# Kernel tuning notes

Hardware: AMD Instinct MI355X
Metric: run time of the kernel (lower is better)

## Reference

```python
import jax, jax.numpy as jnp
import numpy as np

RANK = 16
ALPHA = 32.0


def setup_inputs() -> dict:
    key = jax.random.key(0)
    k1, k2, k3, k4, k5 = jax.random.split(key, 5)
    B_, S, D = 8, 2048, 2048
    x = jax.random.normal(k1, (B_, S, D), dtype=jnp.float32)
    W = jax.random.normal(k2, (D, D), dtype=jnp.float32) * 0.02  # linear.weight [out, in]
    b = jax.random.normal(k3, (D,), dtype=jnp.float32) * 0.02
    # LoRA init: B ~ N(0, 1/rank), A = 0 in the original; use randn*std for both so grads flow
    std = 1.0 / np.sqrt(RANK)
    B = jax.random.normal(k4, (D, RANK), dtype=jnp.float32) * std
    A = jax.random.normal(k5, (RANK, D), dtype=jnp.float32) * 0.02
    return {"x": x, "W": W, "b": b, "B": B, "A": A}


def reference(x, W, b, B, A):
    # delta_w = B @ A  -> [in, out] (== [out, in] since square)
    delta_w = jnp.matmul(B, A)
    w = W + (ALPHA / RANK) * delta_w
    # F.linear(x, w, b) = x @ w.T + b
    return jnp.einsum("bsd,od->bso", x, w) + b
```

## Files before the change

### kernel.cpp

```cpp
#include <hip/hip_runtime.h>
#include <hip/hip_bf16.h>

typedef unsigned short u16;
typedef __bf16 bf16x8 __attribute__((ext_vector_type(8)));
typedef float f32x4 __attribute__((ext_vector_type(4)));

#define MDIM 16384
#define NDIM 2048
#define KDIM 2048
#define RANK 16
#define BM 128
#define BN 128
#define BK 64

#define WPREP_BLOCKS (NDIM * (KDIM / 4) / 256)
#define XCONV_BLOCKS (MDIM * (KDIM / 4) / 256)

__device__ __forceinline__ u16 f2bf(float f) {
    union { float f; unsigned u; } v; v.f = f;
    unsigned u = v.u;
    u += 0x7FFFu + ((u >> 16) & 1u);
    return (u16)(u >> 16);
}

__device__ __forceinline__ void async_copy16(const void* gsrc, void* ldst) {
    __builtin_amdgcn_global_load_lds(
        (const __attribute__((address_space(1))) void*)gsrc,
        (__attribute__((address_space(3))) void*)ldst,
        16, 0, 0);
}

__global__ __launch_bounds__(256) void prep(const float* __restrict__ x,
                                            const float* __restrict__ W,
                                            const float* __restrict__ Bm,
                                            const float* __restrict__ Am,
                                            u16* __restrict__ xb,
                                            u16* __restrict__ wb) {
    const int bid = blockIdx.x;
    if (bid < WPREP_BLOCKS) {
        int t  = bid * 256 + threadIdx.x;
        int o  = t >> 9;
        int dq = t & 511;
        float4 acc = ((const float4*)W)[(size_t)o * (KDIM / 4) + dq];
        const float* Bo = Bm + (size_t)o * RANK;
#pragma unroll
        for (int r = 0; r < RANK; ++r) {
            float bv = 2.0f * Bo[r];
            float4 a4 = ((const float4*)(Am + (size_t)r * KDIM))[dq];
            acc.x += bv * a4.x; acc.y += bv * a4.y;
            acc.z += bv * a4.z; acc.w += bv * a4.w;
        }
        ushort4 ov;
        ov.x = f2bf(acc.x); ov.y = f2bf(acc.y);
        ov.z = f2bf(acc.z); ov.w = f2bf(acc.w);
        ((ushort4*)wb)[t] = ov;
    } else {
        int t = (bid - WPREP_BLOCKS) * 256 + threadIdx.x;
        float4 v = ((const float4*)x)[t];
        ushort4 o;
        o.x = f2bf(v.x); o.y = f2bf(v.y); o.z = f2bf(v.z); o.w = f2bf(v.w);
        ((ushort4*)xb)[t] = o;
    }
}

__global__ __launch_bounds__(256) void gemm_bt(const u16* __restrict__ xb,
                                               const u16* __restrict__ wb,
                                               const float* __restrict__ bias,
                                               float* __restrict__ out) {
    __shared__ __align__(16) u16 As[BM * BK];
    __shared__ __align__(16) u16 Bs[BN * BK];

    const int tid  = threadIdx.x;
    const int lane = tid & 63;
    const int w    = tid >> 6;
    const int m0   = blockIdx.y * BM;
    const int n0   = blockIdx.x * BN;

    const int srow   = lane >> 3;
    const int schunk = (lane & 7) ^ srow;
    const int selem  = schunk * 8;

    const int wr   = (w >> 1) * 64;
    const int wc   = (w & 1) * 64;
    const int quad = lane >> 4;
    const int l16  = lane & 15;
    const int swz  = l16 & 7;

    int a_row[4], b_row[4];
#pragma unroll
    for (int i = 0; i < 4; ++i) {
        a_row[i] = (wr + i * 16 + l16) * BK;
        b_row[i] = (wc + i * 16 + l16) * BK;
    }

    f32x4 acc[4][4];
#pragma unroll
    for (int i = 0; i < 4; ++i)
#pragma unroll
        for (int j = 0; j < 4; ++j)
            acc[i][j] = (f32x4){0.f, 0.f, 0.f, 0.f};

    const u16* ga = xb + (size_t)m0 * KDIM;
    const u16* gb = wb + (size_t)n0 * KDIM;

    for (int k0 = 0; k0 < KDIM; k0 += BK) {
#pragma unroll
        for (int c = 0; c < 4; ++c) {
            const int rbase = w * 32 + c * 8;
            async_copy16(ga + (size_t)(rbase + srow) * KDIM + k0 + selem,
                         (char*)As + (size_t)rbase * (BK * 2));
            async_copy16(gb + (size_t)(rbase + srow) * KDIM + k0 + selem,
                         (char*)Bs + (size_t)rbase * (BK * 2));
        }
        __syncthreads();

#pragma unroll
        for (int s = 0; s < 2; ++s) {
            bf16x8 af[4], bfr[4];
#pragma unroll
            for (int i = 0; i < 4; ++i)
                af[i]  = *(const bf16x8*)(As + a_row[i] + (((s * 4 + quad) ^ swz) << 3));
#pragma unroll
            for (int j = 0; j < 4; ++j)
                bfr[j] = *(const bf16x8*)(Bs + b_row[j] + (((s * 4 + quad) ^ swz) << 3));

#pragma unroll
            for (int i = 0; i < 4; ++i)
#pragma unroll
                for (int j = 0; j < 4; ++j)
                    acc[i][j] = __builtin_amdgcn_mfma_f32_16x16x32_bf16(
                        af[i], bfr[j], acc[i][j], 0, 0, 0);
        }

        __syncthreads();
    }

#pragma unroll
    for (int j = 0; j < 4; ++j) {
        const int col = n0 + wc + j * 16 + l16;
        const float bj = bias[col];
#pragma unroll
        for (int i = 0; i < 4; ++i) {
            const int rowb = m0 + wr + i * 16 + quad * 4;
#pragma unroll
            for (int r = 0; r < 4; ++r)
                out[(size_t)(rowb + r) * NDIM + col] = acc[i][j][r] + bj;
        }
    }
}

extern "C" void kernel_launch(void* const* d_in, const int* in_sizes, int n_in,
                              void* d_out, int out_size, void* d_ws, size_t ws_size,
                              hipStream_t stream) {
    const float* x    = (const float*)d_in[0];
    const float* W    = (const float*)d_in[1];
    const float* bias = (const float*)d_in[2];
    const float* Bm   = (const float*)d_in[3];
    const float* Am   = (const float*)d_in[4];
    float* out = (float*)d_out;

    u16* xb   = (u16*)d_ws;
    u16* wbuf = xb + (size_t)MDIM * KDIM;

    prep<<<WPREP_BLOCKS + XCONV_BLOCKS, 256, 0, stream>>>(x, W, Bm, Am, xb, wbuf);

    dim3 grid(NDIM / BN, MDIM / BM);
    gemm_bt<<<grid, 256, 0, stream>>>(xb, wbuf, bias, out);
}
```

Baseline: 401.0 us.

## Rewrite GEMM with 256x256 tiles, double-buffered LDS pipeline and XCD-aware block mapping

The bf16 GEMM moves from 128x128 tiles with 256 threads and a single LDS buffer to 256x256 tiles with 512 threads (8 waves, each computing 128x64). Global-to-LDS async copies are double-buffered and interleaved with four MFMA phases per K-tile, using explicit barriers, waitcnt and setprio so loads overlap compute. A 1D grid is remapped so consecutive blocks are spread across XCDs for L2 reuse. This removes the load-then-compute stall and raises arithmetic intensity per tile. In exchange it costs more registers and 128KB of LDS per block, and the hand-scheduled waitcnt and barrier ordering is delicate.

```diff
diff --git a/kernel.cpp b/kernel.cpp
--- a/kernel.cpp
+++ b/kernel.cpp
@@ -9,9 +9,11 @@
 #define NDIM 2048
 #define KDIM 2048
 #define RANK 16
-#define BM 128
-#define BN 128
+#define BM 256
+#define BN 256
 #define BK 64
+#define NTILE (KDIM / BK)
+#define NITER (NTILE / 2)
 
 #define WPREP_BLOCKS (NDIM * (KDIM / 4) / 256)
 #define XCONV_BLOCKS (MDIM * (KDIM / 4) / 256)
@@ -63,90 +65,165 @@
     }
 }
 
-__global__ __launch_bounds__(256) void gemm_bt(const u16* __restrict__ xb,
-                                               const u16* __restrict__ wb,
-                                               const float* __restrict__ bias,
-                                               float* __restrict__ out) {
-    __shared__ __align__(16) u16 As[BM * BK];
-    __shared__ __align__(16) u16 Bs[BN * BK];
+__global__ __launch_bounds__(512, 2) void gemm_bt(const u16* __restrict__ xb,
+                                                  const u16* __restrict__ wb,
+                                                  const float* __restrict__ bias,
+                                                  float* __restrict__ out) {
+    __shared__ __align__(16) u16 lds[2][2][BM * BK];
 
     const int tid  = threadIdx.x;
     const int lane = tid & 63;
     const int w    = tid >> 6;
-    const int m0   = blockIdx.y * BM;
-    const int n0   = blockIdx.x * BN;
+    const int wm   = w >> 2;
+    const int wn   = w & 3;
+
+    const int bid = blockIdx.x;
+    const int wg  = (bid & 7) * (512 / 8) + (bid >> 3);
+    const int m0  = (wg >> 3) * BM;
+    const int n0  = (wg & 7) * BN;
 
     const int srow   = lane >> 3;
     const int schunk = (lane & 7) ^ srow;
     const int selem  = schunk * 8;
-
-    const int wr   = (w >> 1) * 64;
-    const int wc   = (w & 1) * 64;
+    const int grow   = w * 8 + srow;
+
     const int quad = lane >> 4;
     const int l16  = lane & 15;
     const int swz  = l16 & 7;
-
-    int a_row[4], b_row[4];
-#pragma unroll
-    for (int i = 0; i < 4; ++i) {
-        a_row[i] = (wr + i * 16 + l16) * BK;
-        b_row[i] = (wc + i * 16 + l16) * BK;
-    }
-
-    f32x4 acc[4][4];
-#pragma unroll
-    for (int i = 0; i < 4; ++i)
+    const int coff0 = ((0 * 4 + quad) ^ swz) << 3;
+    const int coff1 = ((1 * 4 + quad) ^ swz) << 3;
+
+    int arow[8], brow[4];
+#pragma unroll
+    for (int f = 0; f < 8; ++f) arow[f] = (wm * 128 + f * 16 + l16) * BK;
+#pragma unroll
+    for (int j = 0; j < 4; ++j) brow[j] = (wn * 64 + j * 16 + l16) * BK;
+
+    u16* As0 = &lds[0][0][0];
+    u16* Bs0 = &lds[0][1][0];
+    u16* As1 = &lds[1][0][0];
+    u16* Bs1 = &lds[1][1][0];
+
+    const u16* ga = xb + (size_t)m0 * KDIM;
+    const u16* gb = wb + (size_t)n0 * KDIM;
+
+#define STG(dstbase, gsrc, rb, kk)                                             \
+    async_copy16((gsrc) + (size_t)((rb) + grow) * KDIM + (size_t)(kk) + selem, \
+                 (char*)(dstbase) + ((rb) + w * 8) * (BK * 2))
+
+#define BAR do { asm volatile("" ::: "memory");                   \
+                 __builtin_amdgcn_s_barrier();                    \
+                 asm volatile("" ::: "memory"); } while (0)
+#define LGK0 asm volatile("s_waitcnt lgkmcnt(0)" ::: "memory")
+#define VM4  asm volatile("s_waitcnt vmcnt(4)" ::: "memory")
+
+#define LDA_QUAD(base, q)                                                      \
+    _Pragma("unroll")                                                          \
+    for (int i = 0; i < 2; ++i) {                                              \
+        af[i][0] = *(const bf16x8*)((base) + arow[(q) * 2 + i] + coff0);       \
+        af[i][1] = *(const bf16x8*)((base) + arow[(q) * 2 + i] + coff1);       \
+    }
+
+#define LDB_ALL(base)                                                          \
+    _Pragma("unroll")                                                          \
+    for (int j = 0; j < 4; ++j) {                                              \
+        bf[j][0] = *(const bf16x8*)((base) + brow[j] + coff0);                 \
+        bf[j][1] = *(const bf16x8*)((base) + brow[j] + coff1);                 \
+    }
+
+#define MFMA16(q) do {                                                         \
+    __builtin_amdgcn_s_setprio(1);                                             \
+    _Pragma("unroll")                                                          \
+    for (int s = 0; s < 2; ++s)                                                \
+        _Pragma("unroll")                                                      \
+        for (int j = 0; j < 4; ++j)                                            \
+            _Pragma("unroll")                                                  \
+            for (int i = 0; i < 2; ++i)                                        \
+                acc[(q) * 2 + i][j] = __builtin_amdgcn_mfma_f32_16x16x32_bf16( \
+                    af[i][s], bf[j][s], acc[(q) * 2 + i][j], 0, 0, 0);         \
+    __builtin_amdgcn_s_setprio(0);                                             \
+} while (0)
+
+    STG(As0, ga, 0, 0); STG(As0, ga, 64, 0); STG(As0, ga, 128, 0); STG(As0, ga, 192, 0);
+    STG(Bs0, gb, 0, 0); STG(Bs0, gb, 64, 0); STG(Bs0, gb, 128, 0); STG(Bs0, gb, 192, 0);
+    STG(Bs1, gb, 0, BK); STG(Bs1, gb, 64, BK); STG(Bs1, gb, 128, BK); STG(Bs1, gb, 192, BK);
+
+    f32x4 acc[8][4];
+#pragma unroll
+    for (int i = 0; i < 8; ++i)
 #pragma unroll
         for (int j = 0; j < 4; ++j)
             acc[i][j] = (f32x4){0.f, 0.f, 0.f, 0.f};
 
-    const u16* ga = xb + (size_t)m0 * KDIM;
-    const u16* gb = wb + (size_t)n0 * KDIM;
-
-    for (int k0 = 0; k0 < KDIM; k0 += BK) {
-#pragma unroll
-        for (int c = 0; c < 4; ++c) {
-            const int rbase = w * 32 + c * 8;
-            async_copy16(ga + (size_t)(rbase + srow) * KDIM + k0 + selem,
-                         (char*)As + (size_t)rbase * (BK * 2));
-            async_copy16(gb + (size_t)(rbase + srow) * KDIM + k0 + selem,
-                         (char*)Bs + (size_t)rbase * (BK * 2));
+    bf16x8 af[2][2], bf[4][2];
+
+    VM4;
+    BAR;
+
+#pragma unroll 1
+    for (int it = 0; it < NITER; ++it) {
+        const int t   = 2 * it;
+        const int ka1 = (t + 1) * BK;
+        const int kb2 = ((t + 2) & (NTILE - 1)) * BK;
+        const int kb3 = ((t + 3) & (NTILE - 1)) * BK;
+
+        LDB_ALL(Bs0); LDA_QUAD(As0, 0);
+        STG(As1, ga, 0, ka1); STG(As1, ga, 64, ka1);
+        STG(As1, ga, 128, ka1); STG(As1, ga, 192, ka1);
+        BAR; LGK0; MFMA16(0); BAR;
+
+        LDA_QUAD(As0, 1);
+        STG(Bs0, gb, 0, kb2); STG(Bs0, gb, 64, kb2);
+        BAR; LGK0; MFMA16(1); BAR;
+
+        LDA_QUAD(As0, 2);
+        STG(Bs0, gb, 128, kb2); STG(Bs0, gb, 192, kb2);
+        BAR; LGK0; MFMA16(2); BAR;
+
+        LDA_QUAD(As0, 3);
+        BAR; LGK0; MFMA16(3);
+        VM4;
+        BAR;
+
+        LDB_ALL(Bs1); LDA_QUAD(As1, 0);
+        STG(As0, ga, 0, kb2); STG(As0, ga, 64, kb2);
+        STG(As0, ga, 128, kb2); STG(As0, ga, 192, kb2);
+        BAR; LGK0; MFMA16(0); BAR;
+
+        LDA_QUAD(As1, 1);
+        STG(Bs1, gb, 0, kb3); STG(Bs1, gb, 64, kb3);
+        BAR; LGK0; MFMA16(1); BAR;
+
+        LDA_QUAD(As1, 2);
+        STG(Bs1, gb, 128, kb3); STG(Bs1, gb, 192, kb3);
+        BAR; LGK0; MFMA16(2); BAR;
+
+        LDA_QUAD(As1, 3);
+        BAR; LGK0; MFMA16(3);
+        VM4;
+        BAR;
+    }
+
+#pragma unroll
+    for (int j = 0; j < 4; ++j) {
+        const int col = n0 + wn * 64 + j * 16 + l16;
+        const float bj = bias[col];
+#pragma unroll
+        for (int f = 0; f < 8; ++f) {
+            const int rowb = m0 + wm * 128 + f * 16 + quad * 4;
+#pragma unroll
+            for (int r = 0; r < 4; ++r)
+                out[(size_t)(rowb + r) * NDIM + col] = acc[f][j][r] + bj;
         }
-        __syncthreads();
-
-#pragma unroll
-        for (int s = 0; s < 2; ++s) {
-            bf16x8 af[4], bfr[4];
-#pragma unroll
-            for (int i = 0; i < 4; ++i)
-                af[i]  = *(const bf16x8*)(As + a_row[i] + (((s * 4 + quad) ^ swz) << 3));
-#pragma unroll
-            for (int j = 0; j < 4; ++j)
-                bfr[j] = *(const bf16x8*)(Bs + b_row[j] + (((s * 4 + quad) ^ swz) << 3));
-
-#pragma unroll
-            for (int i = 0; i < 4; ++i)
-#pragma unroll
-                for (int j = 0; j < 4; ++j)
-                    acc[i][j] = __builtin_amdgcn_mfma_f32_16x16x32_bf16(
-                        af[i], bfr[j], acc[i][j], 0, 0, 0);
-        }
-
-        __syncthreads();
-    }
-
-#pragma unroll
-    for (int j = 0; j < 4; ++j) {
-        const int col = n0 + wc + j * 16 + l16;
-        const float bj = bias[col];
-#pragma unroll
-        for (int i = 0; i < 4; ++i) {
-            const int rowb = m0 + wr + i * 16 + quad * 4;
-#pragma unroll
-            for (int r = 0; r < 4; ++r)
-                out[(size_t)(rowb + r) * NDIM + col] = acc[i][j][r] + bj;
-        }
-    }
+    }
+
+#undef STG
+#undef BAR
+#undef LGK0
+#undef VM4
+#undef LDA_QUAD
+#undef LDB_ALL
+#undef MFMA16
 }
 
 extern "C" void kernel_launch(void* const* d_in, const int* in_sizes, int n_in,
@@ -164,6 +241,6 @@
 
     prep<<<WPREP_BLOCKS + XCONV_BLOCKS, 256, 0, stream>>>(x, W, Bm, Am, xb, wbuf);
 
-    dim3 grid(NDIM / BN, MDIM / BM);
-    gemm_bt<<<grid, 256, 0, stream>>>(xb, wbuf, bias, out);
-}
+    dim3 grid((MDIM / BM) * (NDIM / BN));
+    gemm_bt<<<grid, 512, 0, stream>>>(xb, wbuf, bias, out);
+}
```

After: 362.4 us. 9.6% less time.
